# Optimization experiments

Hardware: AMD Instinct MI355X
Metric: run time of the kernel (lower is better)

The kernel has to match this reference:

```python
import jax, jax.numpy as jnp
import numpy as np

N = 131072
C = 1000

def setup_inputs() -> dict:
    key = jax.random.key(0)
    k1, k2 = jax.random.split(key)
    input = jax.random.normal(k1, (N, C), dtype=jnp.float32)
    label = jax.random.randint(k2, (N,), 0, C, dtype=jnp.int64)
    return {"input": input, "label": label, "class_num": C}

def reference(input, label, class_num):
    # Original: diag(log(1 + exp(mm(-input, onehot(label)^T))))[i] == log(1 + exp(-input[i, label[i]]))
    # (mm(-input, gt^T)[i, j] = -input[i, label[j]]; diag takes j == i).
    # Collapsed to a per-row gather + stable softplus, then mean over rows.
    picked = jnp.take_along_axis(input, label[:, None], axis=1)[:, 0]  # [N]
    return jnp.mean(jax.nn.softplus(-picked))
```

## Files before the change

kernel.cpp:

```cpp
#include <hip/hip_runtime.h>


#define NBLK 512
#define NTHR 256

__device__ __forceinline__ float block_reduce_sum(float acc) {
    #pragma unroll
    for (int off = 32; off > 0; off >>= 1)
        acc += __shfl_down(acc, off, 64);
    __shared__ float s[NTHR / 64];
    const int lane = threadIdx.x & 63;
    const int wave = threadIdx.x >> 6;
    if (lane == 0) s[wave] = acc;
    __syncthreads();
    float r = 0.f;
    if (threadIdx.x == 0) {
        #pragma unroll
        for (int w = 0; w < NTHR / 64; ++w) r += s[w];
    }
    return r;
}

__global__ void __launch_bounds__(NTHR)
softplus_gather_partial(const float* __restrict__ input,
                        const int* __restrict__ label,
                        float* __restrict__ partial,
                        int N, int C) {
    const int i = blockIdx.x * NTHR + threadIdx.x;
    float acc = 0.f;
    if (i < N) {
        const int lab = label[i];
        const float x = input[(long long)i * C + lab];
        const float z = -x;
        acc = fmaxf(z, 0.f) + log1pf(expf(-fabsf(z)));
    }
    const float b = block_reduce_sum(acc);
    if (threadIdx.x == 0) partial[blockIdx.x] = b;
}

__global__ void __launch_bounds__(NTHR)
final_reduce(const float* __restrict__ partial, float* __restrict__ out,
             float invN) {
    const float2 v = ((const float2*)partial)[threadIdx.x];
    const float r = block_reduce_sum(v.x + v.y);
    if (threadIdx.x == 0) out[0] = r * invN;
}

extern "C" void kernel_launch(void* const* d_in, const int* in_sizes, int n_in,
                              void* d_out, int out_size, void* d_ws, size_t ws_size,
                              hipStream_t stream) {
    const float* input = (const float*)d_in[0];
    const int*   label = (const int*)d_in[1];
    const int N = in_sizes[1];
    const int C = in_sizes[0] / in_sizes[1];
    float* partial = (float*)d_ws;

    softplus_gather_partial<<<NBLK, NTHR, 0, stream>>>(input, label, partial, N, C);
    final_reduce<<<1, NTHR, 0, stream>>>(partial, (float*)d_out, 1.0f / (float)N);
}
```

Before: 11.09 us.

## Process two rows per thread and use per-wave partials with single-wave final reduce

Each thread now handles two rows, loading both labels as an int2 and issuing two independent gathers, with 32-bit offset arithmetic. The block-level shared-memory reduction and its __syncthreads are removed: each wave writes its own partial, giving 1024 partials. The final kernel uses a single wave that sums them with float4 loads. This trades a larger second-stage reduction for less synchronisation and more memory-level parallelism per thread. Unsigned 32-bit offsets hold only because N*C fits in 2^32.

```diff
diff --git a/kernel.cpp b/kernel.cpp
--- a/kernel.cpp
+++ b/kernel.cpp
@@ -1,49 +1,59 @@
 #include <hip/hip_runtime.h>
 
 
-#define NBLK 512
-#define NTHR 256
+#define K1_BLOCKS 256
+#define K1_THREADS 256
+#define ROWS_PER_THREAD 2
+#define NPARTIAL ((K1_BLOCKS * K1_THREADS) / 64)
 
-__device__ __forceinline__ float block_reduce_sum(float acc) {
+__device__ __forceinline__ float wave_reduce(float v) {
     #pragma unroll
     for (int off = 32; off > 0; off >>= 1)
-        acc += __shfl_down(acc, off, 64);
-    __shared__ float s[NTHR / 64];
-    const int lane = threadIdx.x & 63;
-    const int wave = threadIdx.x >> 6;
-    if (lane == 0) s[wave] = acc;
-    __syncthreads();
-    float r = 0.f;
-    if (threadIdx.x == 0) {
-        #pragma unroll
-        for (int w = 0; w < NTHR / 64; ++w) r += s[w];
-    }
-    return r;
+        v += __shfl_down(v, off, 64);
+    return v;
 }
 
-__global__ void __launch_bounds__(NTHR)
+__device__ __forceinline__ float softplus_neg(float x) {
+    const float z = -x;
+    return fmaxf(z, 0.f) + log1pf(expf(-fabsf(z)));
+}
+
+__global__ void __launch_bounds__(K1_THREADS)
 softplus_gather_partial(const float* __restrict__ input,
                         const int* __restrict__ label,
                         float* __restrict__ partial,
                         int N, int C) {
-    const int i = blockIdx.x * NTHR + threadIdx.x;
+    const int gid = blockIdx.x * K1_THREADS + threadIdx.x;
+    const int r0 = gid * ROWS_PER_THREAD;
     float acc = 0.f;
-    if (i < N) {
-        const int lab = label[i];
-        const float x = input[(long long)i * C + lab];
-        const float z = -x;
-        acc = fmaxf(z, 0.f) + log1pf(expf(-fabsf(z)));
+    if (r0 + 1 < N) {
+        const int2 lab = ((const int2*)label)[gid];
+        const unsigned o0 = (unsigned)(r0 * C) + (unsigned)lab.x;
+        const unsigned o1 = (unsigned)(r0 * C) + (unsigned)C + (unsigned)lab.y;
+        const float x0 = input[o0];
+        const float x1 = input[o1];
+        acc = softplus_neg(x0) + softplus_neg(x1);
+    } else {
+        for (int i = r0; i < N; ++i)
+            acc += softplus_neg(input[(long long)i * C + label[i]]);
     }
-    const float b = block_reduce_sum(acc);
-    if (threadIdx.x == 0) partial[blockIdx.x] = b;
+    acc = wave_reduce(acc);
+    if ((threadIdx.x & 63) == 0)
+        partial[gid >> 6] = acc;
 }
 
-__global__ void __launch_bounds__(NTHR)
+__global__ void __launch_bounds__(64)
 final_reduce(const float* __restrict__ partial, float* __restrict__ out,
              float invN) {
-    const float2 v = ((const float2*)partial)[threadIdx.x];
-    const float r = block_reduce_sum(v.x + v.y);
-    if (threadIdx.x == 0) out[0] = r * invN;
+    const float4* p4 = (const float4*)partial;
+    float acc = 0.f;
+    #pragma unroll
+    for (int j = 0; j < 4; ++j) {
+        const float4 v = p4[threadIdx.x + j * 64];
+        acc += (v.x + v.y) + (v.z + v.w);
+    }
+    acc = wave_reduce(acc);
+    if (threadIdx.x == 0) out[0] = acc * invN;
 }
 
 extern "C" void kernel_launch(void* const* d_in, const int* in_sizes, int n_in,
@@ -55,6 +65,7 @@
     const int C = in_sizes[0] / in_sizes[1];
     float* partial = (float*)d_ws;
 
-    softplus_gather_partial<<<NBLK, NTHR, 0, stream>>>(input, label, partial, N, C);
-    final_reduce<<<1, NTHR, 0, stream>>>(partial, (float*)d_out, 1.0f / (float)N);
+    softplus_gather_partial<<<K1_BLOCKS, K1_THREADS, 0, stream>>>(
+        input, label, partial, N, C);
+    final_reduce<<<1, 64, 0, stream>>>(partial, (float*)d_out, 1.0f / (float)N);
 }
```

After: 11.22 us. Within noise of the previous version (+1.1%).
